# Kernel tuning notes

Hardware: AMD Instinct MI355X
Metric: run time of the kernel (lower is better)

## Reference

```python
import jax, jax.numpy as jnp
import numpy as np

B, S, IN, EMB, H = 4, 2048, 256, 512, 8
D = EMB // H
SCALE = 1.0 / np.sqrt(EMB)  # source uses 1/sqrt(embed_size), not head_dim
EPS = 1e-5


def setup_inputs() -> dict:
    key = jax.random.key(0)
    ks = jax.random.split(key, 20)
    def w(k, shape, fan_in):
        return jax.random.normal(k, shape, jnp.float32) * (1.0 / np.sqrt(fan_in))
    inp = {"state_emb": jax.random.normal(ks[0], (B, S, IN), jnp.float32)}
    i = 1
    for p in ("q", "k", "v"):
        inp[f"{p}_W1"] = w(ks[i], (IN, EMB), IN); i += 1
        inp[f"{p}_b1"] = jnp.zeros((EMB,), jnp.float32)
        inp[f"{p}_W2"] = w(ks[i], (EMB, EMB), EMB); i += 1
        inp[f"{p}_b2"] = jnp.zeros((EMB,), jnp.float32)
    inp["f_W1"] = w(ks[i], (EMB, 2 * EMB), EMB); i += 1
    inp["f_b1"] = jnp.zeros((2 * EMB,), jnp.float32)
    inp["f_W2"] = w(ks[i], (2 * EMB, EMB), 2 * EMB); i += 1
    inp["f_b2"] = jnp.zeros((EMB,), jnp.float32)
    inp["ln1_g"] = jnp.ones((EMB,), jnp.float32)
    inp["ln1_b"] = jnp.zeros((EMB,), jnp.float32)
    inp["ln2_g"] = jnp.ones((EMB,), jnp.float32)
    inp["ln2_b"] = jnp.zeros((EMB,), jnp.float32)
    return inp


def _mlp2(x, W1, b1, W2, b2):
    return jax.nn.relu(x @ W1 + b1) @ W2 + b2


def _layernorm(x, g, b):
    mu = jnp.mean(x, axis=-1, keepdims=True)
    var = jnp.mean(jnp.square(x - mu), axis=-1, keepdims=True)
    return (x - mu) * jax.lax.rsqrt(var + EPS) * g + b


def reference(state_emb, q_W1, q_b1, q_W2, q_b2, k_W1, k_b1, k_W2, k_b2,
              v_W1, v_b1, v_W2, v_b2, f_W1, f_b1, f_W2, f_b2,
              ln1_g, ln1_b, ln2_g, ln2_b):
    n, dim = state_emb.shape[0], state_emb.shape[1]
    q = _mlp2(state_emb, q_W1, q_b1, q_W2, q_b2)  # [n, dim, EMB]
    k = _mlp2(state_emb, k_W1, k_b1, k_W2, k_b2)
    v = _mlp2(state_emb, v_W1, v_b1, v_W2, v_b2)
    qh = q.reshape(n, dim, H, D)
    kh = k.reshape(n, dim, H, D)
    vh = v.reshape(n, dim, H, D)
    energy = jnp.einsum('nqhd,nkhd->nhqk', qh, kh)  # [n, H, dim, dim]
    attn = jax.nn.softmax(energy * SCALE, axis=-1)
    ctx = jnp.einsum('nhql,nlhd->nqhd', attn, vh).reshape(n, dim, EMB)
    x = _layernorm(ctx + q, ln1_g, ln1_b)  # residual with queries, per source
    ff = _mlp2(x, f_W1, f_b1, f_W2, f_b2)
    return _layernorm(x + ff, ln2_g, ln2_b)
```

## Files before the change

### kernel.cpp

```cpp
#include <hip/hip_runtime.h>
#include <hip/hip_bf16.h>
#include <math.h>

#define BB   4
#define SS   2048
#define INF_ 256
#define EMB  512
#define NH   8
#define HD   64
#define NT   8192

typedef unsigned short u16;
typedef unsigned int   u32;
typedef __attribute__((ext_vector_type(8))) short bf16x8;
typedef __attribute__((ext_vector_type(8))) unsigned short u16x8;
typedef __attribute__((ext_vector_type(4))) float f32x4;

constexpr float C2  = 0.06375871607f;
constexpr float TB  = 1.00390625f;
constexpr float EPS = 1e-5f;

__device__ __forceinline__ u16 f2bf(float v) {
    __hip_bfloat16 h = __float2bfloat16(v);
    return *(u16*)&h;
}
__device__ __forceinline__ float bf2f(u16 u) {
    __hip_bfloat16 h = *(__hip_bfloat16*)&u;
    return __bfloat162float(h);
}
__device__ __forceinline__ u16 ftrunc_bf(float v) {
    return (u16)(__float_as_uint(v * TB) >> 16);
}
__device__ __forceinline__ f32x4 mfma16(bf16x8 a, bf16x8 b, f32x4 c) {
    return __builtin_amdgcn_mfma_f32_16x16x32_bf16(a, b, c, 0, 0, 0);
}
__device__ __forceinline__ void async16(const void* g, void* l) {
    __builtin_amdgcn_global_load_lds(
        (const __attribute__((address_space(1))) void*)g,
        (__attribute__((address_space(3))) void*)l, 16, 0, 0);
}
__device__ __forceinline__ int derive_flag(const u16* x) {
    const int lane = threadIdx.x & 63;
    const unsigned e = (x[lane * 2] >> 7) & 0xFF;
    float pl = (e == 0 || (e >= 110 && e <= 140)) ? 1.0f : 0.0f;
    #pragma unroll
    for (int o = 1; o < 64; o <<= 1) pl += __shfl_xor(pl, o);
    return pl < 32.0f;
}

__global__ __launch_bounds__(256) void prep(
    const u16* __restrict__ xsrc,
    const void* w0, const void* w1, const void* w2, const void* w3,
    const void* w4, const void* w5, const void* w6, const void* w7,
    const void* p0, const void* p1, const void* p2, const void* p3,
    const void* p4, const void* p5, const void* p6, const void* p7,
    const void* p8, const void* p9, const void* p10, const void* p11,
    u16* __restrict__ xbf, u16* __restrict__ wt1, u16* __restrict__ wt2,
    u16* __restrict__ f1t, u16* __restrict__ f2t, float* __restrict__ small)
{
    const int isf = derive_flag(xsrc);
    const int z = blockIdx.z;
    const int tid = threadIdx.x;

    if (z < 8) {
        int K, M; const void* src; u16* dst;
        switch (z) {
            case 0: K=256;  M=512;  src=w0; dst=wt1;             break;
            case 1: K=256;  M=512;  src=w1; dst=wt1+512*256;     break;
            case 2: K=256;  M=512;  src=w2; dst=wt1+2*512*256;   break;
            case 3: K=512;  M=512;  src=w3; dst=wt2;             break;
            case 4: K=512;  M=512;  src=w4; dst=wt2+512*512;     break;
            case 5: K=512;  M=512;  src=w5; dst=wt2+2*512*512;   break;
            case 6: K=512;  M=1024; src=w6; dst=f1t;             break;
            default:K=1024; M=512;  src=w7; dst=f2t;             break;
        }
        const int m0 = blockIdx.x * 32, k0 = blockIdx.y * 32;
        if (m0 >= M || k0 >= K) return;
        __shared__ u16 t[32][33];
        const int tx = tid & 31, ty = tid >> 5;
        #pragma unroll
        for (int i = 0; i < 4; ++i) {
            const int kk = k0 + ty + i * 8;
            t[ty + i * 8][tx] = isf ? ftrunc_bf(((const float*)src)[(size_t)kk * M + m0 + tx])
                                    : ((const u16*)src)[(size_t)kk * M + m0 + tx];
        }
        __syncthreads();
        #pragma unroll
        for (int i = 0; i < 4; ++i) {
            const int mm = m0 + ty + i * 8;
            dst[(size_t)mm * K + k0 + tx] = t[tx][ty + i * 8];
        }
    } else if (z == 8) {
        const int bid = blockIdx.y * 32 + blockIdx.x;
        const int base = bid * 2048 + tid * 8;
        if (isf) {
            #pragma unroll
            for (int j = 0; j < 8; ++j)
                xbf[base + j] = ftrunc_bf(((const float*)xsrc)[base + j]);
        } else {
            *(u16x8*)&xbf[base] = *(const u16x8*)&xsrc[base];
        }
    } else {
        const int bid = blockIdx.y * 32 + blockIdx.x;
        if (bid >= 28) return;
        const int e = bid * 256 + tid;
        int id, i;
        if (e < 3072)      { id = e >> 9;               i = e & 511;          }
        else if (e < 4096) { id = 6;                    i = e - 3072;         }
        else               { id = 7 + ((e - 4096) >> 9); i = (e - 4096) & 511; }
        const void* src;
        switch (id) {
            case 0: src = p0; break;  case 1: src = p1; break;
            case 2: src = p2; break;  case 3: src = p3; break;
            case 4: src = p4; break;  case 5: src = p5; break;
            case 6: src = p6; break;  case 7: src = p7; break;
            case 8: src = p8; break;  case 9: src = p9; break;
            case 10: src = p10; break; default: src = p11; break;
        }
        small[e] = isf ? ((const float*)src)[i] : bf2f(((const u16*)src)[i]);
    }
}

template <bool RELU, bool AWHICH, bool VOUT, bool SCALEK>
__global__ __launch_bounds__(256) void gemm64(
    const u16* __restrict__ Aall, const u16* __restrict__ Wtall,
    const float* __restrict__ ball, u16* __restrict__ out,
    u16* __restrict__ vtb, int N, int K, int M)
{
    __shared__ __align__(16) u16 sA[64 * 64];
    __shared__ __align__(16) u16 sB[64 * 64];

    const int mtiles = M >> 6;
    const int which = blockIdx.y / mtiles;
    const int colb  = blockIdx.y % mtiles;
    const int row0 = blockIdx.x << 6, col0 = colb << 6;
    const u16* A  = Aall + (AWHICH ? (size_t)which * N * K : 0);
    const u16* Wt = Wtall + (size_t)which * M * K;
    const float* bias = ball + (size_t)which * M;

    const int tid = threadIdx.x;
    const int lane = tid & 63, w = tid >> 6;
    const int wrow = (w & 1) << 5, wcol = (w >> 1) << 5;
    const int c = lane & 15, quad = lane >> 4;

    const u16* ap[2]; const u16* bp[2];
    #pragma unroll
    for (int i = 0; i < 2; ++i) {
        const int raw = i * 256 + tid, r = raw >> 3, ch = (raw & 7) ^ (r & 7);
        ap[i] = A + (size_t)(row0 + r) * K + ch * 8;
        bp[i] = Wt + (size_t)(col0 + r) * K + ch * 8;
    }

    f32x4 acc[2][2] = {};

    for (int k0 = 0; k0 < K; k0 += 64) {
        __syncthreads();
        #pragma unroll
        for (int i = 0; i < 2; ++i) {
            async16(ap[i], (char*)sA + (i * 256 + tid) * 16);
            ap[i] += 64;
            async16(bp[i], (char*)sB + (i * 256 + tid) * 16);
            bp[i] += 64;
        }
        __syncthreads();

        #pragma unroll
        for (int kt = 0; kt < 2; ++kt) {
            bf16x8 af[2], bfr[2];
            #pragma unroll
            for (int rt = 0; rt < 2; ++rt) {
                const int r = wrow + rt * 16 + c;
                af[rt] = *(const bf16x8*)&sA[(r * 8 + ((kt * 4 + quad) ^ (r & 7))) * 8];
            }
            #pragma unroll
            for (int ct = 0; ct < 2; ++ct) {
                const int r = wcol + ct * 16 + c;
                bfr[ct] = *(const bf16x8*)&sB[(r * 8 + ((kt * 4 + quad) ^ (r & 7))) * 8];
            }
            #pragma unroll
            for (int rt = 0; rt < 2; ++rt)
                #pragma unroll
                for (int ct = 0; ct < 2; ++ct)
                    acc[rt][ct] = mfma16(af[rt], bfr[ct], acc[rt][ct]);
        }
    }

    if (VOUT && which == 2) {
        __syncthreads();
        #pragma unroll
        for (int rt = 0; rt < 2; ++rt) {
            const int rowb = wrow + rt * 16 + quad * 4;
            #pragma unroll
            for (int ct = 0; ct < 2; ++ct) {
                const int col = wcol + ct * 16 + c;
                const float bb = bias[col0 + col];
                ushort4 pk;
                pk.x = ftrunc_bf(acc[rt][ct][0] + bb);
                pk.y = ftrunc_bf(acc[rt][ct][1] + bb);
                pk.z = ftrunc_bf(acc[rt][ct][2] + bb);
                pk.w = ftrunc_bf(acc[rt][ct][3] + bb);
                *(ushort4*)&sA[col * 72 + rowb] = pk;
            }
        }
        __syncthreads();
        const int dl = tid >> 2, part = tid & 3;
        const int hg = (col0 + dl) >> 6, dd = (col0 + dl) & 63;
        const int bb = row0 >> 11, s0 = row0 & 2047;
        u16* dst = vtb + ((size_t)(bb * NH + hg) * HD + dd) * SS + s0 + part * 16;
        #pragma unroll
        for (int j = 0; j < 2; ++j)
            *(u16x8*)&dst[j * 8] = *(const u16x8*)&sA[dl * 72 + part * 16 + j * 8];
        return;
    }

    const float sc = (SCALEK && which == 1) ? C2 : 1.0f;
    const size_t outW = (size_t)which * N * M;
    __syncthreads();
    #pragma unroll
    for (int rt = 0; rt < 2; ++rt) {
        #pragma unroll
        for (int ct = 0; ct < 2; ++ct) {
            const int col = wcol + ct * 16 + c;
            const float bb = bias[col0 + col];
            #pragma unroll
            for (int i = 0; i < 4; ++i) {
                const int row = wrow + rt * 16 + quad * 4 + i;
                float v = (acc[rt][ct][i] + bb) * sc;
                if (RELU) v = fmaxf(v, 0.0f);
                sA[row * 72 + col] = ftrunc_bf(v);
            }
        }
    }
    __syncthreads();
    const int dl = tid >> 2, part = tid & 3;
    u16* dst = out + outW + (size_t)(row0 + dl) * M + col0 + part * 16;
    #pragma unroll
    for (int j = 0; j < 2; ++j)
        *(u16x8*)&dst[j * 8] = *(const u16x8*)&sA[dl * 72 + part * 16 + j * 8];
}

__global__ __launch_bounds__(1024) void attn_mfma(
    const u16* __restrict__ q, const u16* __restrict__ k,
    const u16* __restrict__ vt, u16* __restrict__ ctx)
{
    __shared__ __align__(16) u16 sK[2][2][4096];
    __shared__ __align__(16) u16 sV[2][2][4096];
    __shared__ __align__(16) u16 sP[32][1024];

    const int tid = threadIdx.x;
    const int w16 = tid >> 6, lane = tid & 63;
    const int g = w16 >> 3, w = w16 & 7;
    const int c = lane & 15, quad = lane >> 4;
    const int id = blockIdx.x;
    const int slot = id >> 3;
    const int bh = ((id & 7) << 2) | (slot >> 3);
    const int qt = slot & 7;
    const int b = bh >> 3, h = bh & 7;
    const int q0 = qt * 256;
    const size_t tokbase = (size_t)b * SS;
    const int hoff = h * HD;

    bf16x8 qf[2][2];
    #pragma unroll
    for (int f = 0; f < 2; ++f) {
        const int myq = q0 + w * 32 + f * 16 + c;
        #pragma unroll
        for (int kt = 0; kt < 2; ++kt)
            qf[f][kt] = *(const bf16x8*)&q[(tokbase + myq) * EMB + hoff + kt * 32 + quad * 8];
    }

    union { u32 u[4]; bf16x8 v; } ones;
    #pragma unroll
    for (int i = 0; i < 4; ++i) ones.u[i] = 0x3F803F80u;

    const int tig = tid & 511;
    const u16* kp; const u16* vp;
    {
        const int rr = tig >> 3, ch = (tig & 7) ^ (rr & 7);
        kp = k + (tokbase + g * 1024 + rr) * EMB + hoff + ch * 8;
        vp = vt + ((size_t)(b * NH + h) * HD + rr) * SS + g * 1024 + ch * 8;
    }
    auto stage = [&](int buf) {
        async16(kp, (char*)&sK[g][buf][0] + tig * 16);
        kp += 64 * EMB;
        async16(vp, (char*)&sV[g][buf][0] + tig * 16);
        vp += 64;
    };
    stage(0);

    f32x4 accO[2][4] = {};
    f32x4 accL[2] = {};
    const f32x4 zc = {};

    for (int t = 0; t < 16; ++t) {
        __syncthreads();
        const int buf = t & 1;
        if (t + 1 < 16) stage(buf ^ 1);

        f32x4 accS[2][4];
        __builtin_amdgcn_s_setprio(1);
        #pragma unroll
        for (int mt = 0; mt < 4; ++mt) {
            const int key = mt * 16 + c;
            bf16x8 kf0 = *(const bf16x8*)&sK[g][buf][(key * 8 + (quad ^ (key & 7))) * 8];
            #pragma unroll
            for (int f = 0; f < 2; ++f)
                accS[f][mt] = mfma16(kf0, qf[f][0], zc);
            bf16x8 kf1 = *(const bf16x8*)&sK[g][buf][(key * 8 + ((4 + quad) ^ (key & 7))) * 8];
            #pragma unroll
            for (int f = 0; f < 2; ++f)
                accS[f][mt] = mfma16(kf1, qf[f][1], accS[f][mt]);
        }
        __builtin_amdgcn_s_setprio(0);

        #pragma unroll
        for (int f = 0; f < 2; ++f) {
            u32 pw[8];
            #pragma unroll
            for (int mt = 0; mt < 4; ++mt) {
                const float e0 = __builtin_amdgcn_exp2f(accS[f][mt][0]);
                const float e1 = __builtin_amdgcn_exp2f(accS[f][mt][1]);
                const float e2 = __builtin_amdgcn_exp2f(accS[f][mt][2]);
                const float e3 = __builtin_amdgcn_exp2f(accS[f][mt][3]);
                pw[2 * mt]     = __builtin_amdgcn_perm(__float_as_uint(e1), __float_as_uint(e0), 0x07060302u);
                pw[2 * mt + 1] = __builtin_amdgcn_perm(__float_as_uint(e3), __float_as_uint(e2), 0x07060302u);
            }
            #pragma unroll
            for (int mt = 0; mt < 4; ++mt) {
                const int chunkW = 2 * mt + (quad >> 1);
                const int blk = c * 8 + (chunkW ^ (c & 7));
                uint2 u; u.x = pw[2 * mt]; u.y = pw[2 * mt + 1];
                *(uint2*)((char*)&sP[w16 * 2 + f][0] + blk * 16 + 8 * (quad & 1)) = u;
            }
        }

        bf16x8 pf[2][2];
        #pragma unroll
        for (int f = 0; f < 2; ++f) {
            #pragma unroll
            for (int kt = 0; kt < 2; ++kt)
                pf[f][kt] = *(const bf16x8*)&sP[w16 * 2 + f][(c * 8 + ((kt * 4 + quad) ^ (c & 7))) * 8];
        }
        __builtin_amdgcn_s_setprio(1);
        #pragma unroll
        for (int f = 0; f < 2; ++f) {
            accL[f] = mfma16(ones.v, pf[f][0], accL[f]);
            accL[f] = mfma16(ones.v, pf[f][1], accL[f]);
        }
        #pragma unroll
        for (int nt = 0; nt < 4; ++nt) {
            const int d = nt * 16 + c;
            #pragma unroll
            for (int kt = 0; kt < 2; ++kt) {
                bf16x8 vf = *(const bf16x8*)&sV[g][buf][(d * 8 + ((kt * 4 + quad) ^ (d & 7))) * 8];
                #pragma unroll
                for (int f = 0; f < 2; ++f)
                    accO[f][nt] = mfma16(vf, pf[f][kt], accO[f][nt]);
            }
        }
        __builtin_amdgcn_s_setprio(0);
    }

    __syncthreads();
    float* mb = (float*)&sP[0][0];
    float* ml = (float*)&sK[0][0][0];
    if (g == 1) {
        #pragma unroll
        for (int f = 0; f < 2; ++f) {
            const int mtok = w * 32 + f * 16 + c;
            #pragma unroll
            for (int nt = 0; nt < 4; ++nt) {
                const int dcol = (nt * 16 + quad * 4) ^ ((mtok & 7) << 2);
                *(f32x4*)&mb[mtok * 64 + dcol] = accO[f][nt];
            }
            if (quad == 0) ml[mtok] = accL[f][0];
        }
    }
    __syncthreads();
    if (g == 0) {
        #pragma unroll
        for (int f = 0; f < 2; ++f) {
            const int mtok = w * 32 + f * 16 + c;
            const float l = accL[f][0] + ml[mtok];
            const float li = (l > 0.0f) ? (1.0f / l) : 0.0f;
            const int tok = q0 + mtok;
            u16* dst = ctx + (tokbase + tok) * EMB + hoff + quad * 4;
            #pragma unroll
            for (int nt = 0; nt < 4; ++nt) {
                const int dcol = (nt * 16 + quad * 4) ^ ((mtok & 7) << 2);
                const f32x4 pt = *(const f32x4*)&mb[mtok * 64 + dcol];
                ushort4 pk;
                pk.x = ftrunc_bf((accO[f][nt][0] + pt[0]) * li);
                pk.y = ftrunc_bf((accO[f][nt][1] + pt[1]) * li);
                pk.z = ftrunc_bf((accO[f][nt][2] + pt[2]) * li);
                pk.w = ftrunc_bf((accO[f][nt][3] + pt[3]) * li);
                *(ushort4*)&dst[nt * 16] = pk;
            }
        }
    }
}

__global__ __launch_bounds__(256) void ln_mid(
    const u16* __restrict__ a, const u16* __restrict__ b2,
    const float* __restrict__ g, const float* __restrict__ be,
    u16* __restrict__ outb)
{
    const int wave = threadIdx.x >> 6, lane = threadIdx.x & 63;
    const size_t row = (size_t)blockIdx.x * 4 + wave;
    const u16x8 av = *(const u16x8*)&a[row * EMB + lane * 8];
    const u16x8 bv = *(const u16x8*)&b2[row * EMB + lane * 8];
    float vals[8], sum = 0.0f;
    #pragma unroll
    for (int i = 0; i < 8; ++i) { vals[i] = bf2f(av[i]) + bf2f(bv[i]); sum += vals[i]; }
    #pragma unroll
    for (int o = 1; o < 64; o <<= 1) sum += __shfl_xor(sum, o);
    const float mu = sum * (1.0f / 512.0f);
    float vs = 0.0f;
    #pragma unroll
    for (int i = 0; i < 8; ++i) { const float d = vals[i] - mu; vs += d * d; }
    #pragma unroll
    for (int o = 1; o < 64; o <<= 1) vs += __shfl_xor(vs, o);
    const float rstd = rsqrtf(vs * (1.0f / 512.0f) + EPS);
    u16x8 ov;
    #pragma unroll
    for (int i = 0; i < 8; ++i) {
        const int col = lane * 8 + i;
        ov[i] = f2bf((vals[i] - mu) * rstd * g[col] + be[col]);
    }
    *(u16x8*)&outb[row * EMB + lane * 8] = ov;
}

__global__ __launch_bounds__(256) void ln_final(
    const u16* __restrict__ a, const u16* __restrict__ b2,
    const float* __restrict__ g, const float* __restrict__ be,
    void* __restrict__ dout, const u16* __restrict__ xsrc)
{
    const int isf = derive_flag(xsrc);
    const int wave = threadIdx.x >> 6, lane = threadIdx.x & 63;
    const size_t row = (size_t)blockIdx.x * 4 + wave;
    const u16x8 av = *(const u16x8*)&a[row * EMB + lane * 8];
    const u16x8 bv = *(const u16x8*)&b2[row * EMB + lane * 8];
    float vals[8], sum = 0.0f;
    #pragma unroll
    for (int i = 0; i < 8; ++i) { vals[i] = bf2f(av[i]) + bf2f(bv[i]); sum += vals[i]; }
    #pragma unroll
    for (int o = 1; o < 64; o <<= 1) sum += __shfl_xor(sum, o);
    const float mu = sum * (1.0f / 512.0f);
    float vs = 0.0f;
    #pragma unroll
    for (int i = 0; i < 8; ++i) { const float d = vals[i] - mu; vs += d * d; }
    #pragma unroll
    for (int o = 1; o < 64; o <<= 1) vs += __shfl_xor(vs, o);
    const float rstd = rsqrtf(vs * (1.0f / 512.0f) + EPS);
    if (isf) {
        #pragma unroll
        for (int i = 0; i < 8; ++i) {
            const int col = lane * 8 + i;
            ((float*)dout)[row * EMB + col] = (vals[i] - mu) * rstd * g[col] + be[col];
        }
    } else {
        u16x8 ov;
        #pragma unroll
        for (int i = 0; i < 8; ++i) {
            const int col = lane * 8 + i;
            ov[i] = f2bf((vals[i] - mu) * rstd * g[col] + be[col]);
        }
        *(u16x8*)&((u16*)dout)[row * EMB + lane * 8] = ov;
    }
}

extern "C" void kernel_launch(void* const* d_in, const int* in_sizes, int n_in,
                              void* d_out, int out_size, void* d_ws, size_t ws_size,
                              hipStream_t stream)
{
    char* ws = (char*)d_ws;
    float* small = (float*)(ws + 0);
    u16*   wt1   = (u16*)(ws + 32768);
    u16*   wt2   = (u16*)(ws + 819200);
    u16*   f1t   = (u16*)(ws + 2392064);
    u16*   f2t   = (u16*)(ws + 3440640);
    u16*   xbf   = (u16*)(ws + 4489216);
    u16*   h3    = (u16*)(ws + 8683520);
    u16*   qkv   = (u16*)(ws + 33849344);
    u16*   vtb   = (u16*)(ws + 59015168);
    u16*   ctxb  = (u16*)(ws + 67403776);
    u16*   x1b   = (u16*)(ws + 75792384);
    u16*   ffb   = (u16*)(ws + 84180992);

    const dim3 blk(256);
    const u16* xsrc = (const u16*)d_in[0];

    prep<<<dim3(32, 32, 10), blk, 0, stream>>>(
        xsrc,
        d_in[1], d_in[5], d_in[9], d_in[3], d_in[7], d_in[11], d_in[13], d_in[15],
        d_in[2], d_in[6], d_in[10], d_in[4], d_in[8], d_in[12],
        d_in[14], d_in[16], d_in[17], d_in[18], d_in[19], d_in[20],
        xbf, wt1, wt2, f1t, f2t, small);

    gemm64<true, false, false, false><<<dim3(128, 24), blk, 0, stream>>>(
        xbf, wt1, small + 0, h3, nullptr, NT, INF_, EMB);
    gemm64<false, true, true, true><<<dim3(128, 24), blk, 0, stream>>>(
        h3, wt2, small + 1536, qkv, vtb, NT, EMB, EMB);

    attn_mfma<<<dim3(256), dim3(1024), 0, stream>>>(
        qkv, qkv + (size_t)NT * EMB, vtb, ctxb);

    ln_mid<<<NT / 4, blk, 0, stream>>>(ctxb, qkv, small + 4608, small + 5120, x1b);

    u16* h2 = h3;
    gemm64<true, false, false, false><<<dim3(128, 16), blk, 0, stream>>>(
        x1b, f1t, small + 3072, h2, nullptr, NT, EMB, 1024);
    gemm64<false, false, false, false><<<dim3(128, 8), blk, 0, stream>>>(
        h2, f2t, small + 4096, ffb, nullptr, NT, 1024, EMB);

    ln_final<<<NT / 4, blk, 0, stream>>>(x1b, ffb, small + 5632, small + 6144, d_out, xsrc);
}
```

Before: 230.5 us.

## Load V fragments directly from global memory instead of staging through LDS

```diff
diff --git a/kernel.cpp b/kernel.cpp
--- a/kernel.cpp
+++ b/kernel.cpp
@@ -244,7 +244,6 @@
     const u16* __restrict__ vt, u16* __restrict__ ctx)
 {
     __shared__ __align__(16) u16 sK[2][2][4096];
-    __shared__ __align__(16) u16 sV[2][2][4096];
     __shared__ __align__(16) u16 sP[32][1024];
 
     const int tid = threadIdx.x;
@@ -274,19 +273,18 @@
     for (int i = 0; i < 4; ++i) ones.u[i] = 0x3F803F80u;
 
     const int tig = tid & 511;
-    const u16* kp; const u16* vp;
+    const u16* kp;
     {
         const int rr = tig >> 3, ch = (tig & 7) ^ (rr & 7);
         kp = k + (tokbase + g * 1024 + rr) * EMB + hoff + ch * 8;
-        vp = vt + ((size_t)(b * NH + h) * HD + rr) * SS + g * 1024 + ch * 8;
-    }
-    auto stage = [&](int buf) {
+    }
+    auto stageK = [&](int buf) {
         async16(kp, (char*)&sK[g][buf][0] + tig * 16);
         kp += 64 * EMB;
-        async16(vp, (char*)&sV[g][buf][0] + tig * 16);
-        vp += 64;
     };
-    stage(0);
+    stageK(0);
+
+    const u16* vbase = vt + ((size_t)(b * NH + h) * HD + c) * SS + g * 1024 + quad * 8;
 
     f32x4 accO[2][4] = {};
     f32x4 accL[2] = {};
@@ -295,7 +293,13 @@
     for (int t = 0; t < 16; ++t) {
         __syncthreads();
         const int buf = t & 1;
-        if (t + 1 < 16) stage(buf ^ 1);
+
+        bf16x8 vfA[2][2];
+        #pragma unroll
+        for (int nt = 0; nt < 2; ++nt)
+            #pragma unroll
+            for (int kt = 0; kt < 2; ++kt)
+                vfA[nt][kt] = *(const bf16x8*)&vbase[(size_t)(nt * 16) * SS + t * 64 + kt * 32];
 
         f32x4 accS[2][4];
         __builtin_amdgcn_s_setprio(1);
@@ -334,6 +338,15 @@
             }
         }
 
+        bf16x8 vfB[2][2];
+        #pragma unroll
+        for (int nt = 0; nt < 2; ++nt)
+            #pragma unroll
+            for (int kt = 0; kt < 2; ++kt)
+                vfB[nt][kt] = *(const bf16x8*)&vbase[(size_t)((nt + 2) * 16) * SS + t * 64 + kt * 32];
+
+        if (t + 1 < 16) stageK(buf ^ 1);
+
         bf16x8 pf[2][2];
         #pragma unroll
         for (int f = 0; f < 2; ++f) {
@@ -348,14 +361,21 @@
             accL[f] = mfma16(ones.v, pf[f][1], accL[f]);
         }
         #pragma unroll
-        for (int nt = 0; nt < 4; ++nt) {
-            const int d = nt * 16 + c;
+        for (int nt = 0; nt < 2; ++nt) {
             #pragma unroll
             for (int kt = 0; kt < 2; ++kt) {
-                bf16x8 vf = *(const bf16x8*)&sV[g][buf][(d * 8 + ((kt * 4 + quad) ^ (d & 7))) * 8];
                 #pragma unroll
                 for (int f = 0; f < 2; ++f)
-                    accO[f][nt] = mfma16(vf, pf[f][kt], accO[f][nt]);
+                    accO[f][nt] = mfma16(vfA[nt][kt], pf[f][kt], accO[f][nt]);
+            }
+        }
+        #pragma unroll
+        for (int nt = 0; nt < 2; ++nt) {
+            #pragma unroll
+            for (int kt = 0; kt < 2; ++kt) {
+                #pragma unroll
+                for (int f = 0; f < 2; ++f)
+                    accO[f][nt + 2] = mfma16(vfB[nt][kt], pf[f][kt], accO[f][nt + 2]);
             }
         }
         __builtin_amdgcn_s_setprio(0);
```

Measured after the change: 282.6 us. 22.6% more time.
